# Kernel tuning notes

Hardware: AMD Instinct MI355X
Metric: run time of the kernel (lower is better)

Reference implementation:

```python
import jax, jax.numpy as jnp
import numpy as np
import math

D_MODEL = 512
NUM_CLASSES = 8
MEM_SLOTS = 64
STEPS = 4
DECAY = 0.9
TOPK = 8
SCORE_CLIP = 10.0
VOCAB = 32000
MAX_LEN = 2048
B, T = 32, 2048


def _linear_params(key, d_in, d_out):
    kw, kb = jax.random.split(key)
    W = jax.random.normal(kw, (d_in, d_out), jnp.float32) * (1.0 / math.sqrt(d_in))
    b = jnp.zeros((d_out,), jnp.float32)
    return W, b


def setup_inputs() -> dict:
    key = jax.random.key(0)
    ks = jax.random.split(key, 16)
    inp = {}
    inp["input_ids"] = jax.random.randint(ks[0], (B, T), 0, VOCAB)
    inp["attention_mask"] = jnp.ones((B, T), jnp.int32)
    inp["token_emb"] = jax.random.normal(ks[1], (VOCAB, D_MODEL), jnp.float32) * 0.02
    inp["pos_emb"] = jax.random.normal(ks[2], (MAX_LEN, D_MODEL), jnp.float32) * 0.02
    inp["memory_init"] = jax.random.normal(ks[3], (1, MEM_SLOTS, D_MODEL), jnp.float32) * 0.02
    names = ["q", "k", "v", "write", "gate", "rq", "rk", "rv"]
    for i, n in enumerate(names):
        W, b = _linear_params(ks[4 + i], D_MODEL, D_MODEL)
        inp[n + "_W"], inp[n + "_b"] = W, b
    inp["fuse_W"], inp["fuse_b"] = _linear_params(ks[12], 2 * D_MODEL, D_MODEL)
    inp["cls_W"], inp["cls_b"] = _linear_params(ks[13], D_MODEL, NUM_CLASSES)
    inp["tln_g"] = jnp.ones((D_MODEL,), jnp.float32)
    inp["tln_b"] = jnp.zeros((D_MODEL,), jnp.float32)
    inp["mln_g"] = jnp.ones((D_MODEL,), jnp.float32)
    inp["mln_b"] = jnp.zeros((D_MODEL,), jnp.float32)
    return inp


def _layer_norm(x, g, b, eps=1e-5):
    mu = jnp.mean(x, axis=-1, keepdims=True)
    var = jnp.var(x, axis=-1, keepdims=True)
    return (x - mu) * jax.lax.rsqrt(var + eps) * g + b


def _topk_softmax(scores, k):
    # scores: (B, T, S). Equivalent to scatter top-k vals into -inf then softmax:
    # softmax over the top-k entries, zeros elsewhere.
    Bb, Tt, S = scores.shape
    tv, ti = jax.lax.top_k(scores, k)           # (B,T,k)
    w = jax.nn.softmax(tv, axis=-1)
    rows = jnp.arange(Bb * Tt)[:, None]
    out = jnp.zeros((Bb * Tt, S), scores.dtype).at[rows, ti.reshape(-1, k)].set(w.reshape(-1, k))
    return out.reshape(Bb, Tt, S)


def _binding(scores, mask_f, k):
    w = _topk_softmax(jnp.clip(scores, -SCORE_CLIP, SCORE_CLIP), k)
    w = w * mask_f
    return w / jnp.maximum(jnp.sum(w, axis=-1, keepdims=True), 1e-9)


def _forward(input_ids, attention_mask, token_emb, pos_emb, memory_init,
             q_W, q_b, k_W, k_b, v_W, v_b, write_W, write_b, gate_W, gate_b,
             rq_W, rq_b, rk_W, rk_b, rv_W, rv_b, fuse_W, fuse_b,
             cls_W, cls_b, tln_g, tln_b, mln_g, mln_b):
    scale = 1.0 / math.sqrt(D_MODEL)
    tokens = token_emb[input_ids] + pos_emb[jnp.arange(input_ids.shape[1])][None]
    tokens = _layer_norm(tokens, tln_g, tln_b)  # (B,T,D)
    mask_f = attention_mask[..., None].astype(tokens.dtype)  # (B,T,1)
    memory = jnp.broadcast_to(memory_init, (input_ids.shape[0], MEM_SLOTS, D_MODEL))
    for _ in range(STEPS):
        q = tokens @ q_W + q_b
        kk = memory @ k_W + k_b
        scores = jnp.einsum("btd,bsd->bts", q, kk) * scale
        binding = _binding(scores, mask_f, TOPK)  # (B,T,S)
        v = tokens @ v_W + v_b
        write = jnp.einsum("bts,btd->bsd", binding, v)
        slot_usage = jnp.maximum(jnp.sum(binding, axis=1)[..., None], 1e-6)  # (B,S,1)
        write = (write / slot_usage) @ write_W + write_b
        write = jax.nn.sigmoid(write @ gate_W + gate_b) * write
        memory = _layer_norm(DECAY * memory + (1.0 - DECAY) * write, mln_g, mln_b)
    # read
    rq = tokens @ rq_W + rq_b
    rk = memory @ rk_W + rk_b
    rv = memory @ rv_W + rv_b
    scores = jnp.einsum("btd,bsd->bts", rq, rk) * scale
    rw = _binding(scores, mask_f, TOPK)
    context = jnp.einsum("bts,bsd->btd", rw, rv)
    fused = jnp.concatenate([tokens, context], axis=-1) @ fuse_W + fuse_b
    pooled = jnp.sum(fused * mask_f, axis=1) / jnp.maximum(jnp.sum(mask_f, axis=1), 1.0)
    return pooled @ cls_W + cls_b  # (B, C)


def reference(input_ids, attention_mask, token_emb, pos_emb, memory_init,
              q_W, q_b, k_W, k_b, v_W, v_b, write_W, write_b, gate_W, gate_b,
              rq_W, rq_b, rk_W, rk_b, rv_W, rv_b, fuse_W, fuse_b,
              cls_W, cls_b, tln_g, tln_b, mln_g, mln_b):
    return _forward(input_ids, attention_mask, token_emb, pos_emb, memory_init,
                    q_W, q_b, k_W, k_b, v_W, v_b, write_W, write_b, gate_W, gate_b,
                    rq_W, rq_b, rk_W, rk_b, rv_W, rv_b, fuse_W, fuse_b,
                    cls_W, cls_b, tln_g, tln_b, mln_g, mln_b)
```

## Files before the change

kernel.cpp:

```cpp
#include <hip/hip_runtime.h>
#include <hip/hip_bf16.h>
#include <math.h>

#define BB 32
#define TT 2048
#define DM 512
#define SS 64
#define BT (BB*TT)
#define NSTEPS 4
#define SCALE 0.044194173824159216f

typedef unsigned short u16;
typedef unsigned int u32;
typedef __attribute__((ext_vector_type(8))) short s16x8;
typedef __attribute__((ext_vector_type(4))) float f32x4;
typedef __attribute__((ext_vector_type(4))) unsigned u32x4;

__device__ __forceinline__ u16 f2b(float x){
  __hip_bfloat16 h = __float2bfloat16(x);
  return *reinterpret_cast<u16*>(&h);
}
__device__ __forceinline__ float b2f(u16 u){
  __hip_bfloat16 h;
  *reinterpret_cast<u16*>(&h) = u;
  return __bfloat162float(h);
}

static __device__ __forceinline__ float wave_reduce_sum(float v){
  #pragma unroll
  for (int off=32; off; off>>=1) v += __shfl_down(v, off);
  return v;
}

__global__ __launch_bounds__(256) void embed_ln_k(const int* __restrict__ ids,
    const float* __restrict__ temb, const float* __restrict__ pemb,
    const float* __restrict__ g, const float* __restrict__ be, u16* __restrict__ out){
  int row = blockIdx.x*4 + (threadIdx.x>>6);
  int l = threadIdx.x & 63;
  int t = row & (TT-1);
  int id = ids[row];
  const float* te = temb + (size_t)id*DM + l*8;
  const float* pe = pemb + (size_t)t*DM + l*8;
  float4 a0 = *(const float4*)te,     a1 = *(const float4*)(te+4);
  float4 p0 = *(const float4*)pe,     p1 = *(const float4*)(pe+4);
  float x[8] = {a0.x+p0.x, a0.y+p0.y, a0.z+p0.z, a0.w+p0.w,
                a1.x+p1.x, a1.y+p1.y, a1.z+p1.z, a1.w+p1.w};
  float s1 = 0.f, s2 = 0.f;
  #pragma unroll
  for (int e=0;e<8;e++){ s1 += x[e]; s2 += x[e]*x[e]; }
  #pragma unroll
  for (int off=1; off<64; off<<=1){ s1 += __shfl_xor(s1, off); s2 += __shfl_xor(s2, off); }
  float mu = s1*(1.f/DM);
  float var = s2*(1.f/DM) - mu*mu;
  float rs = rsqrtf(var + 1e-5f);
  const float* gp = g + l*8;
  const float* bp = be + l*8;
  float4 g0=*(const float4*)gp, g1=*(const float4*)(gp+4);
  float4 b0=*(const float4*)bp, b1=*(const float4*)(bp+4);
  float gg[8]={g0.x,g0.y,g0.z,g0.w,g1.x,g1.y,g1.z,g1.w};
  float bb[8]={b0.x,b0.y,b0.z,b0.w,b1.x,b1.y,b1.z,b1.w};
  s16x8 o;
  #pragma unroll
  for (int e=0;e<8;e++) o[e] = (short)f2b((x[e]-mu)*rs*gg[e] + bb[e]);
  *(s16x8*)(out + (size_t)row*DM + l*8) = o;
}

template<int EPI>
__global__ __launch_bounds__(128) void ntgemm_k(const u16* __restrict__ A,
    const u16* __restrict__ Bm, const float* __restrict__ bias,
    const u16* __restrict__ mulb, const float* __restrict__ rowv,
    const float* __restrict__ bias2, void* __restrict__ Cout, float scalep){
  int m0 = blockIdx.x*32 + (threadIdx.x>>6)*16;
  int n0 = blockIdx.y*64;
  int l = threadIdx.x & 63;
  int lr = l & 15, lk = (l>>4)*8;
  const u16* Arow = A + (size_t)(m0 + lr)*512 + lk;
  const u16* B0   = Bm + (size_t)(n0 + lr)*512 + lk;
  f32x4 acc[4] = {};
  #pragma unroll
  for (int k0=0;k0<512;k0+=32){
    s16x8 a = *(const s16x8*)(Arow + k0);
    #pragma unroll
    for (int j=0;j<4;j++){
      s16x8 b = *(const s16x8*)(B0 + (size_t)j*16*512 + k0);
      acc[j] = __builtin_amdgcn_mfma_f32_16x16x32_bf16(a, b, acc[j], 0,0,0);
    }
  }
  int mbase = m0 + (l>>4)*4;
  #pragma unroll
  for (int j=0;j<4;j++){
    int n = n0 + j*16 + lr;
    #pragma unroll
    for (int r=0;r<4;r++){
      int m = mbase + r;
      float v = acc[j][r];
      if (EPI==0){ ((u16*)Cout)[(size_t)m*512 + n] = f2b(v + bias[n]); }
      if (EPI==2){
        float z = v + bias[n];
        float sg = 1.f/(1.f + expf(-z));
        ((float*)Cout)[(size_t)m*512 + n] = b2f(mulb[(size_t)m*512 + n]) * sg;
      }
      if (EPI==3){ ((float*)Cout)[(size_t)m*512 + n] = v + bias[n]; }
      if (EPI==4){ ((u16*)Cout)[(size_t)m*512 + n] = f2b(v * scalep); }
      if (EPI==5){ ((u16*)Cout)[(size_t)m*512 + n] = f2b(v + rowv[m]*bias[n] + bias2[n]); }
    }
  }
}

__global__ __launch_bounds__(64) void bind_k(const u16* __restrict__ tok,
    const u16* __restrict__ Pt, const float* __restrict__ cbuf, const int* __restrict__ mask,
    u16* __restrict__ BNDT, float* __restrict__ cspart){
  int b = blockIdx.y, t0 = blockIdx.x*64;
  int l = threadIdx.x;
  int lr = l&15, g = l>>4, lk = g*8;
  __shared__ float sc[64*66];
  __shared__ u16 bt[64*66];

  const u16* Abase = tok + ((size_t)(b*TT + t0 + lr))*512 + lk;
  const u16* Bbase = Pt + ((size_t)(b*SS + lr))*512 + lk;
  f32x4 acc[4][4] = {};
  #pragma unroll
  for (int k0=0;k0<512;k0+=32){
    s16x8 a[4], bb[4];
    #pragma unroll
    for (int mi=0;mi<4;mi++) a[mi] = *(const s16x8*)(Abase + (size_t)mi*16*512 + k0);
    #pragma unroll
    for (int nj=0;nj<4;nj++) bb[nj] = *(const s16x8*)(Bbase + (size_t)nj*16*512 + k0);
    #pragma unroll
    for (int mi=0;mi<4;mi++)
      #pragma unroll
      for (int nj=0;nj<4;nj++)
        acc[mi][nj] = __builtin_amdgcn_mfma_f32_16x16x32_bf16(a[mi], bb[nj], acc[mi][nj], 0,0,0);
  }
  float cbv[4];
  #pragma unroll
  for (int nj=0;nj<4;nj++) cbv[nj] = cbuf[b*SS + 16*nj + lr];
  #pragma unroll
  for (int mi=0;mi<4;mi++)
    #pragma unroll
    for (int nj=0;nj<4;nj++)
      #pragma unroll
      for (int r=0;r<4;r++){
        float x = acc[mi][nj][r] + cbv[nj];
        x = fminf(fmaxf(x, -10.f), 10.f);
        sc[(16*mi + 4*g + r)*66 + 16*nj + lr] = x;
      }

  float sv[64];
  #pragma unroll
  for (int j=0;j<64;j++) sv[j] = sc[l*66 + j];

  u32 work[64];
  #pragma unroll
  for (int j=0;j<64;j++){
    u32 s = __float_as_uint(sv[j]);
    u32 o = s ^ ((u32)(((int)s) >> 31) | 0x80000000u);
    work[j] = (o & 0xFFFFFFC0u) | (u32)(63 - j);
  }
  u32 mtop = 0;
  #pragma unroll
  for (int it=0; it<8; ++it){
    u32 a[32];
    #pragma unroll
    for (int j=0;j<32;j++){ u32 x = work[2*j], y = work[2*j+1]; a[j] = x>y?x:y; }
    #pragma unroll
    for (int lvl=16; lvl>=1; lvl>>=1)
      #pragma unroll
      for (int j=0;j<lvl;j++){ u32 x = a[2*j], y = a[2*j+1]; a[j] = x>y?x:y; }
    u32 m = a[0];
    if (it==0) mtop = m;
    #pragma unroll
    for (int j=0;j<64;j++) work[j] = (work[j]==m) ? 0u : work[j];
  }
  u32 ot = mtop & 0xFFFFFFC0u;
  u32 tb = (ot & 0x80000000u) ? (ot ^ 0x80000000u) : ~ot;
  float T = __uint_as_float(tb);

  float tot = 0.f;
  #pragma unroll
  for (int j=0;j<64;j++){
    float ej = (work[j]==0u) ? expf(sv[j]-T) : 0.f;
    sv[j] = ej;
    tot += ej;
  }
  int mv = mask[b*TT + t0 + l];
  float inv = mv ? 1.f/tot : 0.f;
  #pragma unroll
  for (int j=0;j<64;j++)
    bt[j*66 + l] = f2b(sv[j]*inv);

  const u32* btw = (const u32*)bt;
  u32 rowbuf[32];
  float csum = 0.f;
  #pragma unroll
  for (int w=0;w<32;w++){
    u32 v = btw[l*33 + w];
    rowbuf[w] = v;
    csum += b2f((u16)(v & 0xFFFFu)) + b2f((u16)(v >> 16));
  }
  cspart[((size_t)b*32 + blockIdx.x)*64 + l] = csum;
  u16* dst = BNDT + ((size_t)(b*SS + l))*TT + t0;
  #pragma unroll
  for (int w8=0;w8<8;w8++){
    u32x4 v;
    v[0]=rowbuf[4*w8]; v[1]=rowbuf[4*w8+1]; v[2]=rowbuf[4*w8+2]; v[3]=rowbuf[4*w8+3];
    *(u32x4*)(dst + 8*w8) = v;
  }
}

__global__ __launch_bounds__(64) void csred_k(const float* __restrict__ cspart,
    float* __restrict__ slot, float* __restrict__ rr, float* __restrict__ raw){
  int b = blockIdx.x, s = threadIdx.x;
  float t = 0.f;
  for (int k=0;k<32;k++) t += cspart[((size_t)b*32 + k)*64 + s];
  raw[b*SS+s] = t;
  float sl = fmaxf(t, 1e-6f);
  slot[b*SS+s] = sl;
  rr[b*SS+s] = t/sl;
}

__global__ __launch_bounds__(256) void wt_k(const u16* __restrict__ BNDT,
    const u16* __restrict__ tok, float* __restrict__ part){
  int dgrp = blockIdx.x, b = blockIdx.y, ks = blockIdx.z;
  int tid = threadIdx.x, w = tid>>6, l = tid&63;
  int lr = l&15, lk = (l>>4)*8;
  __shared__ u16 tk[128][72];
  f32x4 acc[8] = {};
  int trow = tid>>2, dseg = (tid&3)*32;
  const u16* tokbase = tok + ((size_t)b*TT)*512 + dgrp*128;
  const u16* Abase = BNDT + ((size_t)(b*SS + 16*w + lr))*TT;
  for (int chunk=0; chunk<8; ++chunk){
    int tb = ks*512 + chunk*64;
    const u16* src = tokbase + (size_t)(tb + trow)*512 + dseg;
    s16x8 v0 = *(const s16x8*)(src);
    s16x8 v1 = *(const s16x8*)(src+8);
    s16x8 v2 = *(const s16x8*)(src+16);
    s16x8 v3 = *(const s16x8*)(src+24);
    #pragma unroll
    for (int e=0;e<8;e++){
      int d0 = dseg+e, d1 = dseg+8+e, d2 = dseg+16+e, d3 = dseg+24+e;
      tk[d0][(trow + 8*((d0>>5)&3)) & 63] = (u16)v0[e];
      tk[d1][(trow + 8*((d1>>5)&3)) & 63] = (u16)v1[e];
      tk[d2][(trow + 8*((d2>>5)&3)) & 63] = (u16)v2[e];
      tk[d3][(trow + 8*((d3>>5)&3)) & 63] = (u16)v3[e];
    }
    __syncthreads();
    #pragma unroll
    for (int kst=0;kst<2;kst++){
      s16x8 a = *(const s16x8*)(Abase + tb + kst*32 + lk);
      #pragma unroll
      for (int nt=0;nt<8;nt++){
        int dd = nt*16 + lr;
        int cb2 = (kst*32 + lk + 8*((dd>>5)&3)) & 63;
        s16x8 bb = *(const s16x8*)&tk[dd][cb2];
        acc[nt] = __builtin_amdgcn_mfma_f32_16x16x32_bf16(a, bb, acc[nt], 0,0,0);
      }
    }
    __syncthreads();
  }
  float* dst = part + (size_t)ks*2048*512 + ((size_t)(b*SS))*512 + dgrp*128;
  #pragma unroll
  for (int nt=0;nt<8;nt++){
    int d = nt*16 + lr;
    #pragma unroll
    for (int r=0;r<4;r++){
      int s = 16*w + (l>>4)*4 + r;
      dst[(size_t)s*512 + d] = acc[nt][r];
    }
  }
}

__global__ __launch_bounds__(256) void wtred_k(const float* __restrict__ part,
    const float* __restrict__ slot, u16* __restrict__ t1h){
  int i = blockIdx.x*256 + threadIdx.x;
  int row = i>>9;
  float v = part[i] + part[i + 2048*512] + part[i + 2*2048*512] + part[i + 3*2048*512];
  t1h[i] = f2b(v / slot[row]);
}

__global__ __launch_bounds__(256) void cb_k(const float* __restrict__ mem,
    const float* __restrict__ wcb, const float* __restrict__ cb0p, float* __restrict__ cb){
  int row = blockIdx.x*4 + (threadIdx.x>>6), l = threadIdx.x&63;
  const float* r = mem + (size_t)row*512;
  float s = 0.f;
  #pragma unroll
  for (int k=0;k<8;k++) s += r[l + 64*k]*wcb[l + 64*k];
  #pragma unroll
  for (int off=32; off; off>>=1) s += __shfl_xor(s, off);
  if (l==0) cb[row] = s + cb0p[0];
}

__global__ __launch_bounds__(256) void matvec_k(const float* __restrict__ W,
    const float* __restrict__ v, float* __restrict__ out){
  int i = blockIdx.x*4 + (threadIdx.x>>6), l = threadIdx.x&63;
  const float* r = W + (size_t)i*512;
  float s = 0.f;
  #pragma unroll
  for (int k=0;k<8;k++) s += r[l + 64*k]*v[l + 64*k];
  #pragma unroll
  for (int off=32; off; off>>=1) s += __shfl_xor(s, off);
  if (l==0) out[i] = s * SCALE;
}

__global__ __launch_bounds__(256) void matvecc_k(const float* __restrict__ W,
    const float* __restrict__ v, float* __restrict__ out){
  int n = blockIdx.x*256 + threadIdx.x;
  float s = 0.f;
  for (int o=0;o<512;o++) s += v[o]*W[(size_t)o*512 + n];
  out[n] = s;
}

__global__ __launch_bounds__(128) void dot2_k(const float* __restrict__ a0, const float* __restrict__ b0,
    const float* __restrict__ a1, const float* __restrict__ b1, float* __restrict__ out){
  int w = threadIdx.x>>6, l = threadIdx.x&63;
  const float* a = w ? a1 : a0;
  const float* b = w ? b1 : b0;
  float s = 0.f;
  #pragma unroll
  for (int k=0;k<8;k++) s += a[l + 64*k]*b[l + 64*k];
  #pragma unroll
  for (int off=32; off; off>>=1) s += __shfl_xor(s, off);
  if (l==0) out[w] = s * SCALE;
}

__global__ __launch_bounds__(256) void tconv_k(const float* __restrict__ in, u16* __restrict__ out){
  __shared__ float t[32][33];
  int c0 = blockIdx.x*32, r0 = blockIdx.y*32;
  int cx = threadIdx.x&31, ry = threadIdx.x>>5;
  #pragma unroll
  for (int i=0;i<4;i++){ int r = ry + i*8; t[r][cx] = in[(size_t)(r0+r)*512 + c0+cx]; }
  __syncthreads();
  #pragma unroll
  for (int i=0;i<4;i++){ int r = ry + i*8; out[(size_t)(c0+r)*512 + r0+cx] = f2b(t[cx][r]); }
}

__global__ __launch_bounds__(256) void conv_k(const float* __restrict__ in, u16* __restrict__ out){
  int i = blockIdx.x*256 + threadIdx.x;
  out[i] = f2b(in[i]);
}

__global__ __launch_bounds__(256) void meminit_k(const float* __restrict__ src,
    float* __restrict__ mem, u16* __restrict__ memh){
  int i = blockIdx.x*256 + threadIdx.x;
  float v = src[i & (SS*DM-1)];
  mem[i] = v;
  memh[i] = f2b(v);
}

__global__ __launch_bounds__(256) void mem_ln_k(float* __restrict__ mem, const float* __restrict__ w3,
    const float* __restrict__ g, const float* __restrict__ be, u16* __restrict__ memh){
  int row = blockIdx.x;
  int d = threadIdx.x;
  float* mrow = mem + (size_t)row*DM;
  const float* wrow = w3 + (size_t)row*DM;
  float x0 = 0.9f*mrow[d]     + 0.1f*wrow[d];
  float x1 = 0.9f*mrow[d+256] + 0.1f*wrow[d+256];
  float s1 = x0+x1, s2 = x0*x0 + x1*x1;
  s1 = wave_reduce_sum(s1); s2 = wave_reduce_sum(s2);
  __shared__ float r1[4], r2[4];
  int lane = d & 63, w = d>>6;
  if (lane==0){ r1[w]=s1; r2[w]=s2; }
  __syncthreads();
  float S1 = r1[0]+r1[1]+r1[2]+r1[3];
  float S2 = r2[0]+r2[1]+r2[2]+r2[3];
  float mu = S1 * (1.f/DM);
  float var = S2*(1.f/DM) - mu*mu;
  float rs = rsqrtf(var + 1e-5f);
  float y0 = (x0-mu)*rs*g[d] + be[d];
  float y1 = (x1-mu)*rs*g[d+256] + be[d+256];
  mrow[d] = y0; mrow[d+256] = y1;
  memh[(size_t)row*DM + d] = f2b(y0);
  memh[(size_t)row*DM + d+256] = f2b(y1);
}

__global__ __launch_bounds__(256) void tokpart_k(const u16* __restrict__ tok,
    const int* __restrict__ mask, float* __restrict__ tp){
  int b = blockIdx.x, sl = blockIdx.y;
  int w = threadIdx.x>>6, l = threadIdx.x&63;
  float acc[8] = {};
  #pragma unroll 4
  for (int i=0;i<32;i++){
    int t = sl*128 + w + 4*i;
    float m = (float)mask[b*TT + t];
    s16x8 v = *(const s16x8*)(tok + ((size_t)(b*TT + t))*512 + l*8);
    #pragma unroll
    for (int e=0;e<8;e++) acc[e] += m*b2f((u16)v[e]);
  }
  float* dst = tp + ((size_t)(b*64 + sl*4 + w))*512 + l*8;
  #pragma unroll
  for (int e=0;e<8;e++) dst[e] = acc[e];
}

__global__ __launch_bounds__(256) void catden_k(const float* __restrict__ tp,
    const float* __restrict__ rws, const float* __restrict__ rv,
    const int* __restrict__ mask, float* __restrict__ cat, float* __restrict__ denomv){
  int b = blockIdx.x, tid = threadIdx.x;
  float dn = 0.f;
  for (int t=tid; t<TT; t+=256) dn += (float)mask[b*TT+t];
  dn = wave_reduce_sum(dn);
  __shared__ float dred[4];
  if ((tid&63)==0) dred[tid>>6]=dn;
  #pragma unroll
  for (int it=0; it<2; ++it){
    int d = tid + it*256;
    float ts = 0.f;
    for (int k=0;k<64;k++) ts += tp[((size_t)(b*64+k))*512 + d];
    cat[(size_t)b*1024 + d] = ts;
    float c = 0.f;
    for (int s=0;s<SS;s++) c += rws[b*SS+s]*rv[((size_t)b*SS+s)*DM + d];
    cat[(size_t)b*1024 + 512 + d] = c;
  }
  __syncthreads();
  if (tid==0) denomv[b] = dred[0]+dred[1]+dred[2]+dred[3];
}

__global__ __launch_bounds__(256) void fuse_k(const float* __restrict__ cat,
    const float* __restrict__ denomv, const float* __restrict__ fuseW,
    const float* __restrict__ fuseb, float* __restrict__ pooled){
  int b = blockIdx.x, n0 = blockIdx.y*64;
  int l = threadIdx.x&63, kc = threadIdx.x>>6;
  int n = n0 + l;
  float acc = 0.f;
  const float* crow = cat + (size_t)b*1024;
  for (int k=kc*256; k<kc*256+256; ++k)
    acc += crow[k]*fuseW[(size_t)k*512 + n];
  __shared__ float red[4][64];
  red[kc][l] = acc;
  __syncthreads();
  if (kc==0){
    float denom = denomv[b];
    float tot = red[0][l]+red[1][l]+red[2][l]+red[3][l];
    pooled[(size_t)b*512 + n] = (tot + denom*fuseb[n]) / fmaxf(denom, 1.f);
  }
}

__global__ __launch_bounds__(256) void cls_k(const float* __restrict__ pooled,
    const float* __restrict__ clsW, const float* __restrict__ clsb, float* __restrict__ out){
  int b = blockIdx.x;
  int c = threadIdx.x&7, kc = threadIdx.x>>3;
  float acc = 0.f;
  const float* prow = pooled + (size_t)b*512;
  for (int d=kc*16; d<kc*16+16; ++d) acc += prow[d]*clsW[d*8+c];
  __shared__ float red[32][8];
  red[kc][c] = acc;
  __syncthreads();
  if (threadIdx.x < 8){
    float tot = 0.f;
    #pragma unroll
    for (int k=0;k<32;k++) tot += red[k][threadIdx.x];
    out[b*8 + threadIdx.x] = tot + clsb[threadIdx.x];
  }
}

extern "C" void kernel_launch(void* const* d_in, const int* in_sizes, int n_in,
                              void* d_out, int out_size, void* d_ws, size_t ws_size,
                              hipStream_t stream){
  (void)in_sizes; (void)n_in; (void)out_size; (void)ws_size;
  const int*   ids   = (const int*)d_in[0];
  const int*   amask = (const int*)d_in[1];
  const float* temb  = (const float*)d_in[2];
  const float* pemb  = (const float*)d_in[3];
  const float* mem0  = (const float*)d_in[4];
  const float* qW=(const float*)d_in[5],  *qB=(const float*)d_in[6];
  const float* kW=(const float*)d_in[7],  *kB=(const float*)d_in[8];
  const float* vW=(const float*)d_in[9],  *vB=(const float*)d_in[10];
  const float* wrW=(const float*)d_in[11],*wrB=(const float*)d_in[12];
  const float* gtW=(const float*)d_in[13],*gtB=(const float*)d_in[14];
  const float* rqW=(const float*)d_in[15],*rqB=(const float*)d_in[16];
  const float* rkW=(const float*)d_in[17],*rkB=(const float*)d_in[18];
  const float* rvW=(const float*)d_in[19],*rvB=(const float*)d_in[20];
  const float* fW=(const float*)d_in[21], *fB=(const float*)d_in[22];
  const float* cW=(const float*)d_in[23], *cB=(const float*)d_in[24];
  const float* tg=(const float*)d_in[25], *tb=(const float*)d_in[26];
  const float* mg=(const float*)d_in[27], *mb=(const float*)d_in[28];

  char* p = (char*)d_ws;
  size_t off = 0;
  auto alloc = [&](size_t bytes)->char*{ char* r = p + off; off += (bytes + 255) & ~(size_t)255; return r; };
  u16*   tokens = (u16*)  alloc((size_t)BT*DM*2);
  u16*   Pt     = (u16*)  alloc((size_t)BB*SS*DM*2);
  u16*   BNDT   = (u16*)  alloc((size_t)BB*SS*TT*2);
  float* cspart = (float*)alloc((size_t)BB*32*64*4);
  float* wtpart = (float*)alloc((size_t)4*2048*512*4);
  u16*   t1h    = (u16*)  alloc((size_t)2048*512*2);
  u16*   zh     = (u16*)  alloc((size_t)2048*512*2);
  float* mem    = (float*)alloc((size_t)BB*SS*DM*4);
  u16*   memh   = (u16*)  alloc((size_t)BB*SS*DM*2);
  u16*   wrWT   = (u16*)  alloc(512*512*2);
  u16*   gtWT   = (u16*)  alloc(512*512*2);
  u16*   rvWT   = (u16*)  alloc(512*512*2);
  u16*   WqkT   = (u16*)  alloc(512*512*2);
  u16*   WqkT_r = (u16*)  alloc(512*512*2);
  u16*   WvwT   = (u16*)  alloc(512*512*2);
  float* bq     = (float*)alloc(512*4);
  float* bq_r   = (float*)alloc(512*4);
  float* wcb    = (float*)alloc(512*4);
  float* wcb_r  = (float*)alloc(512*4);
  float* bvw    = (float*)alloc(512*4);
  float* cb0s   = (float*)alloc(256);
  float* cbuf   = (float*)alloc(2048*4);
  float* slot   = (float*)alloc(2048*4);
  float* rr     = (float*)alloc(2048*4);
  float* raw    = (float*)alloc(2048*4);
  float* catbuf = (float*)alloc((size_t)BB*1024*4);
  float* denomv = (float*)alloc(BB*4);
  float* pooled = (float*)alloc((size_t)BB*512*4);
  float* rv32   = wtpart;
  float* tspart = wtpart + 1048576;
  float* gh32   = wtpart + 2097152;
  u16*   qWb    = (u16*)((char*)wtpart + 12582912);
  u16*   kWb    = qWb + 512*512;
  u16*   rqWb   = kWb + 512*512;
  u16*   rkWb   = rqWb + 512*512;
  u16*   vWb    = (u16*)((char*)wtpart + 14680064);

  conv_k<<<1024, 256, 0, stream>>>(qW, qWb);
  conv_k<<<1024, 256, 0, stream>>>(kW, kWb);
  conv_k<<<1024, 256, 0, stream>>>(rqW, rqWb);
  conv_k<<<1024, 256, 0, stream>>>(rkW, rkWb);
  conv_k<<<1024, 256, 0, stream>>>(vW, vWb);
  tconv_k<<<dim3(16,16), 256, 0, stream>>>(wrW, wrWT);
  tconv_k<<<dim3(16,16), 256, 0, stream>>>(gtW, gtWT);
  tconv_k<<<dim3(16,16), 256, 0, stream>>>(rvW, rvWT);
  ntgemm_k<4><<<dim3(16,8), 128, 0, stream>>>(qWb, kWb, nullptr, nullptr, nullptr, nullptr, WqkT, SCALE);
  ntgemm_k<4><<<dim3(16,8), 128, 0, stream>>>(rqWb, rkWb, nullptr, nullptr, nullptr, nullptr, WqkT_r, SCALE);
  ntgemm_k<4><<<dim3(16,8), 128, 0, stream>>>(wrWT, vWb, nullptr, nullptr, nullptr, nullptr, WvwT, 1.0f);
  matvec_k<<<128, 256, 0, stream>>>(qW, kB, bq);
  matvec_k<<<128, 256, 0, stream>>>(rqW, rkB, bq_r);
  matvec_k<<<128, 256, 0, stream>>>(kW, qB, wcb);
  matvec_k<<<128, 256, 0, stream>>>(rkW, rqB, wcb_r);
  matvecc_k<<<2, 256, 0, stream>>>(wrW, vB, bvw);
  dot2_k<<<1, 128, 0, stream>>>(kB, qB, rkB, rqB, cb0s);
  embed_ln_k<<<BT/4, 256, 0, stream>>>(ids, temb, pemb, tg, tb, tokens);
  meminit_k<<<(BB*SS*DM)/256, 256, 0, stream>>>(mem0, mem, memh);

  for (int step=0; step<NSTEPS; ++step){
    ntgemm_k<0><<<dim3(64,8), 128, 0, stream>>>(memh, WqkT, bq, nullptr, nullptr, nullptr, Pt, 0.f);
    cb_k<<<512, 256, 0, stream>>>(mem, wcb, cb0s, cbuf);
    bind_k<<<dim3(32,32), 64, 0, stream>>>(tokens, Pt, cbuf, amask, BNDT, cspart);
    csred_k<<<32, 64, 0, stream>>>(cspart, slot, rr, raw);
    wt_k<<<dim3(4,32,4), 256, 0, stream>>>(BNDT, tokens, wtpart);
    wtred_k<<<4096, 256, 0, stream>>>(wtpart, slot, t1h);
    ntgemm_k<5><<<dim3(64,8), 128, 0, stream>>>(t1h, WvwT, bvw, nullptr, rr, wrB, zh, 0.f);
    ntgemm_k<2><<<dim3(64,8), 128, 0, stream>>>(zh, gtWT, gtB, zh, nullptr, nullptr, gh32, 0.f);
    mem_ln_k<<<BB*SS, 256, 0, stream>>>(mem, gh32, mg, mb, memh);
  }

  ntgemm_k<0><<<dim3(64,8), 128, 0, stream>>>(memh, WqkT_r, bq_r, nullptr, nullptr, nullptr, Pt, 0.f);
  cb_k<<<512, 256, 0, stream>>>(mem, wcb_r, cb0s+1, cbuf);
  bind_k<<<dim3(32,32), 64, 0, stream>>>(tokens, Pt, cbuf, amask, BNDT, cspart);
  csred_k<<<32, 64, 0, stream>>>(cspart, slot, rr, raw);
  ntgemm_k<3><<<dim3(64,8), 128, 0, stream>>>(memh, rvWT, rvB, nullptr, nullptr, nullptr, rv32, 0.f);
  tokpart_k<<<dim3(32,16), 256, 0, stream>>>(tokens, amask, tspart);
  catden_k<<<32, 256, 0, stream>>>(tspart, raw, rv32, amask, catbuf, denomv);
  fuse_k<<<dim3(32,8), 256, 0, stream>>>(catbuf, denomv, fW, fB, pooled);
  cls_k<<<32, 256, 0, stream>>>(pooled, cW, cB, (float*)d_out);
}
```

Before: 586.1 us.

## Batch setup launches, fuse Pt GEMM with cb, and drop split-K in wt

The many small setup kernels (conversions, transposes, weight-product GEMMs, matvecs) are merged into a few multi-purpose launches selected by block index. The per-step Pt GEMM and the cb row-dot kernel now run as one launch. The split-K wt kernel plus its reduction pass is replaced by a single kernel that loops over all of T and writes normalized bf16 directly. This removes launch overhead and a 16MB partial-buffer round trip, but the wt grid drops from 512 to 256 blocks, each running a longer serial loop, which may reduce parallelism.

```diff
diff --git a/kernel.cpp b/kernel.cpp
--- a/kernel.cpp
+++ b/kernel.cpp
@@ -94,15 +94,57 @@
     for (int r=0;r<4;r++){
       int m = mbase + r;
       float v = acc[j][r];
-      if (EPI==0){ ((u16*)Cout)[(size_t)m*512 + n] = f2b(v + bias[n]); }
       if (EPI==2){
         float z = v + bias[n];
         float sg = 1.f/(1.f + expf(-z));
         ((float*)Cout)[(size_t)m*512 + n] = b2f(mulb[(size_t)m*512 + n]) * sg;
       }
       if (EPI==3){ ((float*)Cout)[(size_t)m*512 + n] = v + bias[n]; }
-      if (EPI==4){ ((u16*)Cout)[(size_t)m*512 + n] = f2b(v * scalep); }
       if (EPI==5){ ((u16*)Cout)[(size_t)m*512 + n] = f2b(v + rowv[m]*bias[n] + bias2[n]); }
+    }
+  }
+}
+
+__global__ __launch_bounds__(128) void ptcb_k(const u16* __restrict__ A,
+    const u16* __restrict__ Bm, const float* __restrict__ bias,
+    const float* __restrict__ mem, const float* __restrict__ wcb,
+    const float* __restrict__ cb0p, u16* __restrict__ Pt, float* __restrict__ cb){
+  int l = threadIdx.x & 63;
+  if (blockIdx.y < 8){
+    int m0 = blockIdx.x*32 + (threadIdx.x>>6)*16;
+    int n0 = blockIdx.y*64;
+    int lr = l & 15, lk = (l>>4)*8;
+    const u16* Arow = A + (size_t)(m0 + lr)*512 + lk;
+    const u16* B0   = Bm + (size_t)(n0 + lr)*512 + lk;
+    f32x4 acc[4] = {};
+    #pragma unroll
+    for (int k0=0;k0<512;k0+=32){
+      s16x8 a = *(const s16x8*)(Arow + k0);
+      #pragma unroll
+      for (int j=0;j<4;j++){
+        s16x8 b = *(const s16x8*)(B0 + (size_t)j*16*512 + k0);
+        acc[j] = __builtin_amdgcn_mfma_f32_16x16x32_bf16(a, b, acc[j], 0,0,0);
+      }
+    }
+    int mbase = m0 + (l>>4)*4;
+    #pragma unroll
+    for (int j=0;j<4;j++){
+      int n = n0 + j*16 + lr;
+      #pragma unroll
+      for (int r=0;r<4;r++)
+        Pt[(size_t)(mbase+r)*512 + n] = f2b(acc[j][r] + bias[n]);
+    }
+  } else {
+    int base = blockIdx.x*32 + (threadIdx.x>>6)*16;
+    for (int i=0;i<16;i++){
+      int row = base + i;
+      const float* r = mem + (size_t)row*512;
+      float s = 0.f;
+      #pragma unroll
+      for (int k=0;k<8;k++) s += r[l + 64*k]*wcb[l + 64*k];
+      #pragma unroll
+      for (int off=32; off; off>>=1) s += __shfl_xor(s, off);
+      if (l==0) cb[row] = s + cb0p[0];
     }
   }
 }
@@ -219,111 +261,72 @@
   rr[b*SS+s] = t/sl;
 }
 
-__global__ __launch_bounds__(256) void wt_k(const u16* __restrict__ BNDT,
-    const u16* __restrict__ tok, float* __restrict__ part){
-  int dgrp = blockIdx.x, b = blockIdx.y, ks = blockIdx.z;
+__global__ __launch_bounds__(256) void wtfused_k(const u16* __restrict__ BNDT,
+    const u16* __restrict__ tok, const float* __restrict__ slot, u16* __restrict__ t1h){
+  int dgrp = blockIdx.x, b = blockIdx.y;
   int tid = threadIdx.x, w = tid>>6, l = tid&63;
   int lr = l&15, lk = (l>>4)*8;
-  __shared__ u16 tk[128][72];
-  f32x4 acc[8] = {};
-  int trow = tid>>2, dseg = (tid&3)*32;
-  const u16* tokbase = tok + ((size_t)b*TT)*512 + dgrp*128;
+  __shared__ u16 tk[64][72];
+  f32x4 acc[4] = {};
+  int trow = tid>>2, dcol = (tid&3)*16;
+  const u16* tokbase = tok + ((size_t)b*TT)*512 + dgrp*64;
   const u16* Abase = BNDT + ((size_t)(b*SS + 16*w + lr))*TT;
-  for (int chunk=0; chunk<8; ++chunk){
-    int tb = ks*512 + chunk*64;
-    const u16* src = tokbase + (size_t)(tb + trow)*512 + dseg;
+  for (int tb=0; tb<TT; tb+=64){
+    const u16* src = tokbase + (size_t)(tb + trow)*512 + dcol;
     s16x8 v0 = *(const s16x8*)(src);
     s16x8 v1 = *(const s16x8*)(src+8);
-    s16x8 v2 = *(const s16x8*)(src+16);
-    s16x8 v3 = *(const s16x8*)(src+24);
     #pragma unroll
     for (int e=0;e<8;e++){
-      int d0 = dseg+e, d1 = dseg+8+e, d2 = dseg+16+e, d3 = dseg+24+e;
-      tk[d0][(trow + 8*((d0>>5)&3)) & 63] = (u16)v0[e];
-      tk[d1][(trow + 8*((d1>>5)&3)) & 63] = (u16)v1[e];
-      tk[d2][(trow + 8*((d2>>5)&3)) & 63] = (u16)v2[e];
-      tk[d3][(trow + 8*((d3>>5)&3)) & 63] = (u16)v3[e];
+      int d0 = dcol+e, d1 = dcol+8+e;
+      tk[d0][(trow + 8*((d0>>5)&1)) & 63] = (u16)v0[e];
+      tk[d1][(trow + 8*((d1>>5)&1)) & 63] = (u16)v1[e];
     }
     __syncthreads();
     #pragma unroll
     for (int kst=0;kst<2;kst++){
       s16x8 a = *(const s16x8*)(Abase + tb + kst*32 + lk);
       #pragma unroll
-      for (int nt=0;nt<8;nt++){
+      for (int nt=0;nt<4;nt++){
         int dd = nt*16 + lr;
-        int cb2 = (kst*32 + lk + 8*((dd>>5)&3)) & 63;
+        int cb2 = (kst*32 + lk + 8*((dd>>5)&1)) & 63;
         s16x8 bb = *(const s16x8*)&tk[dd][cb2];
         acc[nt] = __builtin_amdgcn_mfma_f32_16x16x32_bf16(a, bb, acc[nt], 0,0,0);
       }
     }
     __syncthreads();
   }
-  float* dst = part + (size_t)ks*2048*512 + ((size_t)(b*SS))*512 + dgrp*128;
-  #pragma unroll
-  for (int nt=0;nt<8;nt++){
-    int d = nt*16 + lr;
+  #pragma unroll
+  for (int nt=0;nt<4;nt++){
+    int d = dgrp*64 + nt*16 + lr;
     #pragma unroll
     for (int r=0;r<4;r++){
       int s = 16*w + (l>>4)*4 + r;
-      dst[(size_t)s*512 + d] = acc[nt][r];
-    }
-  }
-}
-
-__global__ __launch_bounds__(256) void wtred_k(const float* __restrict__ part,
-    const float* __restrict__ slot, u16* __restrict__ t1h){
-  int i = blockIdx.x*256 + threadIdx.x;
-  int row = i>>9;
-  float v = part[i] + part[i + 2048*512] + part[i + 2*2048*512] + part[i + 3*2048*512];
-  t1h[i] = f2b(v / slot[row]);
-}
-
-__global__ __launch_bounds__(256) void cb_k(const float* __restrict__ mem,
-    const float* __restrict__ wcb, const float* __restrict__ cb0p, float* __restrict__ cb){
-  int row = blockIdx.x*4 + (threadIdx.x>>6), l = threadIdx.x&63;
-  const float* r = mem + (size_t)row*512;
-  float s = 0.f;
-  #pragma unroll
-  for (int k=0;k<8;k++) s += r[l + 64*k]*wcb[l + 64*k];
-  #pragma unroll
-  for (int off=32; off; off>>=1) s += __shfl_xor(s, off);
-  if (l==0) cb[row] = s + cb0p[0];
-}
-
-__global__ __launch_bounds__(256) void matvec_k(const float* __restrict__ W,
-    const float* __restrict__ v, float* __restrict__ out){
-  int i = blockIdx.x*4 + (threadIdx.x>>6), l = threadIdx.x&63;
-  const float* r = W + (size_t)i*512;
-  float s = 0.f;
-  #pragma unroll
-  for (int k=0;k<8;k++) s += r[l + 64*k]*v[l + 64*k];
-  #pragma unroll
-  for (int off=32; off; off>>=1) s += __shfl_xor(s, off);
-  if (l==0) out[i] = s * SCALE;
-}
-
-__global__ __launch_bounds__(256) void matvecc_k(const float* __restrict__ W,
-    const float* __restrict__ v, float* __restrict__ out){
-  int n = blockIdx.x*256 + threadIdx.x;
-  float s = 0.f;
-  for (int o=0;o<512;o++) s += v[o]*W[(size_t)o*512 + n];
-  out[n] = s;
-}
-
-__global__ __launch_bounds__(128) void dot2_k(const float* __restrict__ a0, const float* __restrict__ b0,
-    const float* __restrict__ a1, const float* __restrict__ b1, float* __restrict__ out){
-  int w = threadIdx.x>>6, l = threadIdx.x&63;
-  const float* a = w ? a1 : a0;
-  const float* b = w ? b1 : b0;
-  float s = 0.f;
-  #pragma unroll
-  for (int k=0;k<8;k++) s += a[l + 64*k]*b[l + 64*k];
-  #pragma unroll
-  for (int off=32; off; off>>=1) s += __shfl_xor(s, off);
-  if (l==0) out[w] = s * SCALE;
-}
-
-__global__ __launch_bounds__(256) void tconv_k(const float* __restrict__ in, u16* __restrict__ out){
+      int row = b*64 + s;
+      t1h[(size_t)row*512 + d] = f2b(acc[nt][r] / slot[row]);
+    }
+  }
+}
+
+__global__ __launch_bounds__(256) void allconv_k(
+    const float* __restrict__ s0, u16* __restrict__ d0,
+    const float* __restrict__ s1, u16* __restrict__ d1,
+    const float* __restrict__ s2, u16* __restrict__ d2,
+    const float* __restrict__ s3, u16* __restrict__ d3,
+    const float* __restrict__ s4, u16* __restrict__ d4){
+  int sel = blockIdx.x >> 10;
+  int i = (blockIdx.x & 1023)*256 + threadIdx.x;
+  const float* s; u16* d;
+  if (sel==0){s=s0;d=d0;} else if (sel==1){s=s1;d=d1;} else if (sel==2){s=s2;d=d2;}
+  else if (sel==3){s=s3;d=d3;} else {s=s4;d=d4;}
+  d[i] = f2b(s[i]);
+}
+
+__global__ __launch_bounds__(256) void alltconv_k(
+    const float* __restrict__ s0, u16* __restrict__ d0,
+    const float* __restrict__ s1, u16* __restrict__ d1,
+    const float* __restrict__ s2, u16* __restrict__ d2){
+  const float* in; u16* out;
+  if (blockIdx.z==0){in=s0;out=d0;} else if (blockIdx.z==1){in=s1;out=d1;} else {in=s2;out=d2;}
   __shared__ float t[32][33];
   int c0 = blockIdx.x*32, r0 = blockIdx.y*32;
   int cx = threadIdx.x&31, ry = threadIdx.x>>5;
@@ -334,9 +337,81 @@
   for (int i=0;i<4;i++){ int r = ry + i*8; out[(size_t)(c0+r)*512 + r0+cx] = f2b(t[cx][r]); }
 }
 
-__global__ __launch_bounds__(256) void conv_k(const float* __restrict__ in, u16* __restrict__ out){
-  int i = blockIdx.x*256 + threadIdx.x;
-  out[i] = f2b(in[i]);
+__global__ __launch_bounds__(128) void pregemm_k(
+    const u16* __restrict__ A0, const u16* __restrict__ B0, u16* __restrict__ C0, float p0,
+    const u16* __restrict__ A1, const u16* __restrict__ B1, u16* __restrict__ C1, float p1,
+    const u16* __restrict__ A2, const u16* __restrict__ B2, u16* __restrict__ C2, float p2){
+  const u16* A; const u16* Bm; u16* C; float sp;
+  if (blockIdx.z==0){A=A0;Bm=B0;C=C0;sp=p0;}
+  else if (blockIdx.z==1){A=A1;Bm=B1;C=C1;sp=p1;}
+  else {A=A2;Bm=B2;C=C2;sp=p2;}
+  int m0 = blockIdx.x*32 + (threadIdx.x>>6)*16;
+  int n0 = blockIdx.y*64;
+  int l = threadIdx.x & 63;
+  int lr = l & 15, lk = (l>>4)*8;
+  const u16* Arow = A + (size_t)(m0 + lr)*512 + lk;
+  const u16* Bp   = Bm + (size_t)(n0 + lr)*512 + lk;
+  f32x4 acc[4] = {};
+  #pragma unroll
+  for (int k0=0;k0<512;k0+=32){
+    s16x8 a = *(const s16x8*)(Arow + k0);
+    #pragma unroll
+    for (int j=0;j<4;j++){
+      s16x8 b = *(const s16x8*)(Bp + (size_t)j*16*512 + k0);
+      acc[j] = __builtin_amdgcn_mfma_f32_16x16x32_bf16(a, b, acc[j], 0,0,0);
+    }
+  }
+  int mbase = m0 + (l>>4)*4;
+  #pragma unroll
+  for (int j=0;j<4;j++){
+    int n = n0 + j*16 + lr;
+    #pragma unroll
+    for (int r=0;r<4;r++)
+      C[(size_t)(mbase+r)*512 + n] = f2b(acc[j][r] * sp);
+  }
+}
+
+__global__ __launch_bounds__(256) void smalls_k(
+    const float* __restrict__ qW, const float* __restrict__ kB, float* __restrict__ bq,
+    const float* __restrict__ rqW, const float* __restrict__ rkB, float* __restrict__ bq_r,
+    const float* __restrict__ kW, const float* __restrict__ qB, float* __restrict__ wcb,
+    const float* __restrict__ rkW, const float* __restrict__ rqB, float* __restrict__ wcb_r,
+    const float* __restrict__ wrW, const float* __restrict__ vB, float* __restrict__ bvw,
+    float* __restrict__ cb0s){
+  int blk = blockIdx.x;
+  if (blk < 512){
+    int which = blk >> 7;
+    const float* W; const float* v; float* out;
+    if (which==0){W=qW; v=kB; out=bq;}
+    else if (which==1){W=rqW; v=rkB; out=bq_r;}
+    else if (which==2){W=kW; v=qB; out=wcb;}
+    else {W=rkW; v=rqB; out=wcb_r;}
+    int i = (blk&127)*4 + (threadIdx.x>>6), l = threadIdx.x&63;
+    const float* r = W + (size_t)i*512;
+    float s = 0.f;
+    #pragma unroll
+    for (int k=0;k<8;k++) s += r[l + 64*k]*v[l + 64*k];
+    #pragma unroll
+    for (int off=32; off; off>>=1) s += __shfl_xor(s, off);
+    if (l==0) out[i] = s * SCALE;
+  } else if (blk < 514){
+    int n = (blk-512)*256 + threadIdx.x;
+    float s = 0.f;
+    for (int o=0;o<512;o++) s += vB[o]*wrW[(size_t)o*512 + n];
+    bvw[n] = s;
+  } else {
+    if (threadIdx.x < 128){
+      int w = threadIdx.x>>6, l = threadIdx.x&63;
+      const float* a = w ? rkB : kB;
+      const float* bvec = w ? rqB : qB;
+      float s = 0.f;
+      #pragma unroll
+      for (int k=0;k<8;k++) s += a[l + 64*k]*bvec[l + 64*k];
+      #pragma unroll
+      for (int off=32; off; off>>=1) s += __shfl_xor(s, off);
+      if (l==0) cb0s[w] = s * SCALE;
+    }
+  }
 }
 
 __global__ __launch_bounds__(256) void meminit_k(const float* __restrict__ src,
@@ -481,7 +556,7 @@
   u16*   Pt     = (u16*)  alloc((size_t)BB*SS*DM*2);
   u16*   BNDT   = (u16*)  alloc((size_t)BB*SS*TT*2);
   float* cspart = (float*)alloc((size_t)BB*32*64*4);
-  float* wtpart = (float*)alloc((size_t)4*2048*512*4);
+  float* scratch= (float*)alloc((size_t)4*2048*512*4);
   u16*   t1h    = (u16*)  alloc((size_t)2048*512*2);
   u16*   zh     = (u16*)  alloc((size_t)2048*512*2);
   float* mem    = (float*)alloc((size_t)BB*SS*DM*4);
@@ -505,49 +580,36 @@
   float* catbuf = (float*)alloc((size_t)BB*1024*4);
   float* denomv = (float*)alloc(BB*4);
   float* pooled = (float*)alloc((size_t)BB*512*4);
-  float* rv32   = wtpart;
-  float* tspart = wtpart + 1048576;
-  float* gh32   = wtpart + 2097152;
-  u16*   qWb    = (u16*)((char*)wtpart + 12582912);
+  float* rv32   = scratch;
+  float* tspart = scratch + 1048576;
+  float* gh32   = scratch + 2097152;
+  u16*   qWb    = (u16*)((char*)scratch + 12582912);
   u16*   kWb    = qWb + 512*512;
   u16*   rqWb   = kWb + 512*512;
   u16*   rkWb   = rqWb + 512*512;
-  u16*   vWb    = (u16*)((char*)wtpart + 14680064);
-
-  conv_k<<<1024, 256, 0, stream>>>(qW, qWb);
-  conv_k<<<1024, 256, 0, stream>>>(kW, kWb);
-  conv_k<<<1024, 256, 0, stream>>>(rqW, rqWb);
-  conv_k<<<1024, 256, 0, stream>>>(rkW, rkWb);
-  conv_k<<<1024, 256, 0, stream>>>(vW, vWb);
-  tconv_k<<<dim3(16,16), 256, 0, stream>>>(wrW, wrWT);
-  tconv_k<<<dim3(16,16), 256, 0, stream>>>(gtW, gtWT);
-  tconv_k<<<dim3(16,16), 256, 0, stream>>>(rvW, rvWT);
-  ntgemm_k<4><<<dim3(16,8), 128, 0, stream>>>(qWb, kWb, nullptr, nullptr, nullptr, nullptr, WqkT, SCALE);
-  ntgemm_k<4><<<dim3(16,8), 128, 0, stream>>>(rqWb, rkWb, nullptr, nullptr, nullptr, nullptr, WqkT_r, SCALE);
-  ntgemm_k<4><<<dim3(16,8), 128, 0, stream>>>(wrWT, vWb, nullptr, nullptr, nullptr, nullptr, WvwT, 1.0f);
-  matvec_k<<<128, 256, 0, stream>>>(qW, kB, bq);
-  matvec_k<<<128, 256, 0, stream>>>(rqW, rkB, bq_r);
-  matvec_k<<<128, 256, 0, stream>>>(kW, qB, wcb);
-  matvec_k<<<128, 256, 0, stream>>>(rkW, rqB, wcb_r);
-  matvecc_k<<<2, 256, 0, stream>>>(wrW, vB, bvw);
-  dot2_k<<<1, 128, 0, stream>>>(kB, qB, rkB, rqB, cb0s);
+  u16*   vWb    = (u16*)((char*)scratch + 14680064);
+
+  allconv_k<<<5120, 256, 0, stream>>>(qW, qWb, kW, kWb, rqW, rqWb, rkW, rkWb, vW, vWb);
+  alltconv_k<<<dim3(16,16,3), 256, 0, stream>>>(wrW, wrWT, gtW, gtWT, rvW, rvWT);
+  pregemm_k<<<dim3(16,8,3), 128, 0, stream>>>(qWb, kWb, WqkT, SCALE,
+                                              rqWb, rkWb, WqkT_r, SCALE,
+                                              wrWT, vWb, WvwT, 1.0f);
+  smalls_k<<<515, 256, 0, stream>>>(qW, kB, bq, rqW, rkB, bq_r, kW, qB, wcb,
+                                    rkW, rqB, wcb_r, wrW, vB, bvw, cb0s);
   embed_ln_k<<<BT/4, 256, 0, stream>>>(ids, temb, pemb, tg, tb, tokens);
   meminit_k<<<(BB*SS*DM)/256, 256, 0, stream>>>(mem0, mem, memh);
 
   for (int step=0; step<NSTEPS; ++step){
-    ntgemm_k<0><<<dim3(64,8), 128, 0, stream>>>(memh, WqkT, bq, nullptr, nullptr, nullptr, Pt, 0.f);
-    cb_k<<<512, 256, 0, stream>>>(mem, wcb, cb0s, cbuf);
+    ptcb_k<<<dim3(64,9), 128, 0, stream>>>(memh, WqkT, bq, mem, wcb, cb0s, Pt, cbuf);
     bind_k<<<dim3(32,32), 64, 0, stream>>>(tokens, Pt, cbuf, amask, BNDT, cspart);
     csred_k<<<32, 64, 0, stream>>>(cspart, slot, rr, raw);
-    wt_k<<<dim3(4,32,4), 256, 0, stream>>>(BNDT, tokens, wtpart);
-    wtred_k<<<4096, 256, 0, stream>>>(wtpart, slot, t1h);
+    wtfused_k<<<dim3(8,32), 256, 0, stream>>>(BNDT, tokens, slot, t1h);
     ntgemm_k<5><<<dim3(64,8), 128, 0, stream>>>(t1h, WvwT, bvw, nullptr, rr, wrB, zh, 0.f);
     ntgemm_k<2><<<dim3(64,8), 128, 0, stream>>>(zh, gtWT, gtB, zh, nullptr, nullptr, gh32, 0.f);
     mem_ln_k<<<BB*SS, 256, 0, stream>>>(mem, gh32, mg, mb, memh);
   }
 
-  ntgemm_k<0><<<dim3(64,8), 128, 0, stream>>>(memh, WqkT_r, bq_r, nullptr, nullptr, nullptr, Pt, 0.f);
-  cb_k<<<512, 256, 0, stream>>>(mem, wcb_r, cb0s+1, cbuf);
+  ptcb_k<<<dim3(64,9), 128, 0, stream>>>(memh, WqkT_r, bq_r, mem, wcb_r, cb0s+1, Pt, cbuf);
   bind_k<<<dim3(32,32), 64, 0, stream>>>(tokens, Pt, cbuf, amask, BNDT, cspart);
   csred_k<<<32, 64, 0, stream>>>(cspart, slot, rr, raw);
   ntgemm_k<3><<<dim3(64,8), 128, 0, stream>>>(memh, rvWT, rvB, nullptr, nullptr, nullptr, rv32, 0.f);
```

Result: slower. 624.5 us (+6.6%).
